# Optimization experiments

Hardware: AMD Instinct MI355X
Metric: run time of the kernel (lower is better)

## Reference

```python
import jax, jax.numpy as jnp
import numpy as np

B, D, H, W = 32, 64, 32, 32   # batch, laten_dim, latent spatial dims
K = 2048                      # codebook_size


def setup_inputs() -> dict:
    key = jax.random.key(0)
    k1, k2 = jax.random.split(key)
    laten = jax.random.normal(k1, (B, D, H, W), dtype=jnp.float32)
    codebook = jax.random.normal(k2, (K, D), dtype=jnp.float32)
    return {"laten": laten, "codebook": codebook}


def reference(laten, codebook):
    # Faithful jax translation of VQVAE.quant_laten.
    b, c, h, w = laten.shape
    # (b, c, h, w) -> (b*h*w, c)
    x = jnp.transpose(laten, (0, 2, 3, 1)).reshape(-1, c)  # (N, D)
    # avoids materializing the (N, K, D) broadcast intermediate.
    x_sq = jnp.sum(x * x, axis=-1, keepdims=True)          # (N, 1)
    e_sq = jnp.sum(codebook * codebook, axis=-1)           # (K,)
    l2_distance = (x_sq - 2.0 * (x @ codebook.T) + e_sq) / c  # (N, K)
    closest_idx_2d = jnp.argmin(l2_distance, axis=-1).reshape(b, h, w)
    # gather + permute(0, 3, 1, 2)
    quant_laten = jnp.transpose(codebook[closest_idx_2d], (0, 3, 1, 2))
    return closest_idx_2d, quant_laten
```

## Files before the change

### kernel.cpp

```cpp
#include <hip/hip_runtime.h>

#define N_PIX 32768
#define DIM   64
#define KCODE 2048

typedef __attribute__((ext_vector_type(8))) short bf16x8;
typedef __attribute__((ext_vector_type(4))) float f32x4;

__device__ inline unsigned short f2bf(float v) {
    unsigned int u = __float_as_uint(v);
    return (unsigned short)((u + 0x7FFFu + ((u >> 16) & 1u)) >> 16);
}
__device__ inline float bf2f(unsigned short b) {
    return __uint_as_float(((unsigned int)b) << 16);
}

__global__ __launch_bounds__(256)
void convert_b_kernel(const float* __restrict__ cb, unsigned short* __restrict__ Bg,
                      float* __restrict__ esq) {
    const int t   = blockIdx.x * 256 + threadIdx.x;
    const int n   = t >> 4;
    const int sub = t & 15;
    const int ntile = n >> 4, ni = n & 15;

    const float4 v = *(const float4*)(cb + (size_t)n * DIM + sub * 4);

    unsigned int h01, h23, m01, m23, l01, l23;
    {
        unsigned short h, m, l;
        float r1;
        h = f2bf(v.x); r1 = v.x - bf2f(h); m = f2bf(r1); l = f2bf(r1 - bf2f(m));
        h01 = h;       m01 = m;       l01 = l;
        h = f2bf(v.y); r1 = v.y - bf2f(h); m = f2bf(r1); l = f2bf(r1 - bf2f(m));
        h01 |= (unsigned int)h << 16; m01 |= (unsigned int)m << 16; l01 |= (unsigned int)l << 16;
        h = f2bf(v.z); r1 = v.z - bf2f(h); m = f2bf(r1); l = f2bf(r1 - bf2f(m));
        h23 = h;       m23 = m;       l23 = l;
        h = f2bf(v.w); r1 = v.w - bf2f(h); m = f2bf(r1); l = f2bf(r1 - bf2f(m));
        h23 |= (unsigned int)h << 16; m23 |= (unsigned int)m << 16; l23 |= (unsigned int)l << 16;
    }

    float s = (v.x * v.x + v.y * v.y) + (v.z * v.z + v.w * v.w);
#pragma unroll
    for (int mk = 1; mk < 16; mk <<= 1) s += __shfl_xor(s, mk, 16);
    if (sub == 0) esq[n] = s;

    char* outb = (char*)Bg;
    const size_t u = ((((size_t)ntile) * 8 + (sub >> 1)) << 8) + ni * 16 + (sub & 1) * 8;
    uint2 hw2 = {h01, h23}, mw2 = {m01, m23}, lw2 = {l01, l23};
    *(uint2*)(outb + u)          = hw2;
    *(uint2*)(outb + 262144 + u) = mw2;
    *(uint2*)(outb + 524288 + u) = lw2;
}

#define DO_PASS(APL, BPL)                                                    \
    _Pragma("unroll") for (int ks = 0; ks < 2; ++ks)                         \
    _Pragma("unroll") for (int mt = 0; mt < 2; ++mt)                         \
        acc[mt] = __builtin_amdgcn_mfma_f32_16x16x32_bf16(                   \
            af[APL][mt][ks], bfr[BPL][ks], acc[mt], 0, 0, 0);

#define LOAD_BFR(PL)                                                         \
    _Pragma("unroll") for (int ks = 0; ks < 2; ++ks)                         \
        bfr[PL][ks] = *(const bf16x8*)(rb + (PL) * 8192 + ks * 1024 + lane * 16);

__device__ __forceinline__ void stage_unit(const char* BgB, char* ringBase,
                                           int u, int it, int slotOff, int lane) {
    const int pl = u >> 3, rem = u & 7, g = rem >> 1, ks = rem & 1;
    const char* gsrc = BgB + (size_t)pl * 262144 + (size_t)(g * 32 + it) * 2048
                     + ks * 1024 + lane * 16;
    char* ldst = ringBase + slotOff + pl * 8192 + g * 2048 + ks * 1024;
    __builtin_amdgcn_global_load_lds(
        (const __attribute__((address_space(1))) void*)gsrc,
        (__attribute__((address_space(3))) void*)ldst, 16, 0, 0);
}

__global__ __launch_bounds__(512, 4)
void dist_fused_kernel(const float* __restrict__ laten,
                       const unsigned short* __restrict__ Bg,
                       const float* __restrict__ esq,
                       const float* __restrict__ cb,
                       float* __restrict__ out0, float* __restrict__ out1) {
    __shared__ __align__(16) char ring[49152];
    __shared__ float esqS[2048];

    const int tid  = threadIdx.x;
    const int lane = tid & 63;
    const int wave = tid >> 6;
    const int wm   = wave & 1;
    const int wn   = wave >> 1;
    const int quad = lane >> 4, col = lane & 15;
    const int bx = blockIdx.x;
    const int bb = bx >> 4, hw0 = (bx & 15) * 64;

    const char* BgB = (const char*)Bg;

    {
        const int p = tid & 63, dg = tid >> 6;
        const float* srcA = laten + (size_t)bb * 65536 + (size_t)dg * 8192 + hw0 + p;
        const int mt = p >> 4, mi = p & 15;
        alignas(16) unsigned short hv[8], mv[8], lv[8];
#pragma unroll
        for (int j = 0; j < 8; ++j) {
            float v = srcA[(size_t)j << 10];
            unsigned short h = f2bf(v);
            float r1 = v - bf2f(h);
            unsigned short m = f2bf(r1);
            unsigned short l = f2bf(r1 - bf2f(m));
            hv[j] = h; mv[j] = m; lv[j] = l;
        }
        int u = ((mt * 8 + dg) << 8) + mi * 16;
        *(uint4*)(ring + u)         = *(uint4*)hv;
        *(uint4*)(ring + 8192 + u)  = *(uint4*)mv;
        *(uint4*)(ring + 16384 + u) = *(uint4*)lv;
    }
    *(float4*)(esqS + tid * 4) = *(const float4*)(esq + tid * 4);
    __syncthreads();

    bf16x8 af[3][2][2];
#pragma unroll
    for (int pl = 0; pl < 3; ++pl)
#pragma unroll
        for (int mt = 0; mt < 2; ++mt)
#pragma unroll
            for (int ks = 0; ks < 2; ++ks)
                af[pl][mt][ks] = *(const bf16x8*)(ring + pl * 8192
                    + (((wm * 2 + mt) * 8 + ks * 4 + quad) << 8) + col * 16);
    __syncthreads();

    stage_unit(BgB, ring, wave,      0, 0, lane);
    stage_unit(BgB, ring, wave + 8,  0, 0, lane);
    stage_unit(BgB, ring, wave + 16, 0, 0, lane);
    __syncthreads();

    float best[2][4];
    int   bidx[2][4];
#pragma unroll
    for (int mt = 0; mt < 2; ++mt)
#pragma unroll
        for (int r = 0; r < 4; ++r) { best[mt][r] = 3.4e38f; bidx[mt][r] = 0; }

    for (int it = 0; it < 32; ++it) {
        if (it < 31) {
            const int slotOff = ((it + 1) & 1) * 24576;
            stage_unit(BgB, ring, wave,      it + 1, slotOff, lane);
            stage_unit(BgB, ring, wave + 8,  it + 1, slotOff, lane);
            stage_unit(BgB, ring, wave + 16, it + 1, slotOff, lane);
        }

        const char* rb = ring + (it & 1) * 24576 + wn * 2048;
        bf16x8 bfr[3][2];
        LOAD_BFR(2)
        LOAD_BFR(0)
        LOAD_BFR(1)

        f32x4 acc[2];
#pragma unroll
        for (int mt = 0; mt < 2; ++mt) acc[mt] = {0.f, 0.f, 0.f, 0.f};

        DO_PASS(0, 2)
        DO_PASS(2, 0)
        DO_PASS(1, 1)
        DO_PASS(0, 1)
        DO_PASS(1, 0)
        DO_PASS(0, 0)

        const int n = wn * 512 + it * 16 + col;
        const float e = esqS[n];
#pragma unroll
        for (int mt = 0; mt < 2; ++mt)
#pragma unroll
            for (int r = 0; r < 4; ++r) {
                float d = fmaf(-2.f, acc[mt][r], e);
                if (d < best[mt][r]) { best[mt][r] = d; bidx[mt][r] = n; }
            }

        __syncthreads();
    }

    float* redD = (float*)ring;
    int*   redI = (int*)(ring + 1024);
    int*   idxF = (int*)(ring + 2048);
#pragma unroll
    for (int mt = 0; mt < 2; ++mt)
#pragma unroll
        for (int r = 0; r < 4; ++r) {
            float d = best[mt][r];
            int   i = bidx[mt][r];
#pragma unroll
            for (int m = 1; m < 16; m <<= 1) {
                float od = __shfl_xor(d, m, 16);
                int   oi = __shfl_xor(i, m, 16);
                if (od < d || (od == d && oi < i)) { d = od; i = oi; }
            }
            if (col == 0) {
                int row = wm * 32 + mt * 16 + quad * 4 + r;
                redD[row * 4 + wn] = d;
                redI[row * 4 + wn] = i;
            }
        }
    __syncthreads();

    if (tid < 64) {
        float bd = redD[tid * 4]; int bi = redI[tid * 4];
#pragma unroll
        for (int w = 1; w < 4; ++w) {
            float d = redD[tid * 4 + w]; int i = redI[tid * 4 + w];
            if (d < bd || (d == bd && i < bi)) { bd = d; bi = i; }
        }
        out0[bx * 64 + tid] = (float)bi;
        idxF[tid] = bi;
    }
    __syncthreads();

    const int p = tid & 63, dg = tid >> 6;
    const int idx = idxF[p];
    const float4* srcr = (const float4*)(cb + ((size_t)idx << 6) + dg * 8);
    float* o = out1 + (size_t)bb * 65536 + (size_t)dg * 8192 + hw0 + p;
    float4 v0 = srcr[0], v1 = srcr[1];
    o[(size_t)0 << 10] = v0.x; o[(size_t)1 << 10] = v0.y;
    o[(size_t)2 << 10] = v0.z; o[(size_t)3 << 10] = v0.w;
    o[(size_t)4 << 10] = v1.x; o[(size_t)5 << 10] = v1.y;
    o[(size_t)6 << 10] = v1.z; o[(size_t)7 << 10] = v1.w;
}

extern "C" void kernel_launch(void* const* d_in, const int* in_sizes, int n_in,
                              void* d_out, int out_size, void* d_ws, size_t ws_size,
                              hipStream_t stream) {
    const float* laten = (const float*)d_in[0];
    const float* cb    = (const float*)d_in[1];

    float* out0 = (float*)d_out;
    float* out1 = (float*)d_out + N_PIX;

    float* esq = (float*)d_ws;
    unsigned short* Bg = (unsigned short*)(esq + 2048);

    convert_b_kernel<<<128, 256, 0, stream>>>(cb, Bg, esq);

    dist_fused_kernel<<<512, 512, 0, stream>>>(laten, Bg, esq, cb, out0, out1);
}
```

Baseline: 103.3 us.

## Triple-buffer codebook LDS ring with vmcnt waits and MFMA priority

Expands the LDS staging ring from two to three slots and prefetches two iterations ahead. Each iteration now waits only on the older async global-to-LDS loads with a partial vmcnt instead of a full barrier drain, and raises wave priority around the MFMA block. The goal is to hide global load latency behind matrix work. LDS per block grows from about 56KB to 80KB, which may lower the number of blocks resident per CU.

```diff
diff --git a/kernel.cpp b/kernel.cpp
--- a/kernel.cpp
+++ b/kernel.cpp
@@ -73,13 +73,52 @@
         (__attribute__((address_space(3))) void*)ldst, 16, 0, 0);
 }
 
+#define ITER(J, DOSTAGE, VM)                                                 \
+  {                                                                          \
+    if (DOSTAGE) {                                                           \
+      const int so2 = (((J) + 2) % 3) * 24576;                               \
+      stage_unit(BgB, ring, wave,      (J) + 2, so2, lane);                  \
+      stage_unit(BgB, ring, wave + 8,  (J) + 2, so2, lane);                  \
+      stage_unit(BgB, ring, wave + 16, (J) + 2, so2, lane);                  \
+    }                                                                        \
+    asm volatile("s_waitcnt vmcnt(" #VM ")" ::: "memory");                   \
+    __builtin_amdgcn_s_barrier();                                            \
+    asm volatile("" ::: "memory");                                           \
+    const char* rb = ring + (((J) % 3) * 24576) + wn * 2048;                 \
+    bf16x8 bfr[3][2];                                                        \
+    LOAD_BFR(2)                                                              \
+    LOAD_BFR(0)                                                              \
+    LOAD_BFR(1)                                                              \
+    f32x4 acc[2];                                                            \
+    acc[0] = f32x4{0.f, 0.f, 0.f, 0.f};                                      \
+    acc[1] = f32x4{0.f, 0.f, 0.f, 0.f};                                      \
+    __builtin_amdgcn_s_setprio(1);                                           \
+    DO_PASS(0, 2)                                                            \
+    DO_PASS(2, 0)                                                            \
+    DO_PASS(1, 1)                                                            \
+    DO_PASS(0, 1)                                                            \
+    DO_PASS(1, 0)                                                            \
+    DO_PASS(0, 0)                                                            \
+    __builtin_amdgcn_s_setprio(0);                                           \
+    const int n = wn * 512 + (J) * 16 + col;                                 \
+    const float e = esqS[n];                                                 \
+    _Pragma("unroll") for (int mt = 0; mt < 2; ++mt)                         \
+    _Pragma("unroll") for (int r = 0; r < 4; ++r) {                          \
+      float d = fmaf(-2.f, acc[mt][r], e);                                   \
+      if (d < best[mt][r]) { best[mt][r] = d; bidx[mt][r] = n; }             \
+    }                                                                        \
+    asm volatile("s_waitcnt lgkmcnt(0)" ::: "memory");                       \
+    __builtin_amdgcn_s_barrier();                                            \
+    asm volatile("" ::: "memory");                                           \
+  }
+
 __global__ __launch_bounds__(512, 4)
 void dist_fused_kernel(const float* __restrict__ laten,
                        const unsigned short* __restrict__ Bg,
                        const float* __restrict__ esq,
                        const float* __restrict__ cb,
                        float* __restrict__ out0, float* __restrict__ out1) {
-    __shared__ __align__(16) char ring[49152];
+    __shared__ __align__(16) char ring[73728];
     __shared__ float esqS[2048];
 
     const int tid  = threadIdx.x;
@@ -129,7 +168,9 @@
     stage_unit(BgB, ring, wave,      0, 0, lane);
     stage_unit(BgB, ring, wave + 8,  0, 0, lane);
     stage_unit(BgB, ring, wave + 16, 0, 0, lane);
-    __syncthreads();
+    stage_unit(BgB, ring, wave,      1, 24576, lane);
+    stage_unit(BgB, ring, wave + 8,  1, 24576, lane);
+    stage_unit(BgB, ring, wave + 16, 1, 24576, lane);
 
     float best[2][4];
     int   bidx[2][4];
@@ -138,43 +179,9 @@
 #pragma unroll
         for (int r = 0; r < 4; ++r) { best[mt][r] = 3.4e38f; bidx[mt][r] = 0; }
 
-    for (int it = 0; it < 32; ++it) {
-        if (it < 31) {
-            const int slotOff = ((it + 1) & 1) * 24576;
-            stage_unit(BgB, ring, wave,      it + 1, slotOff, lane);
-            stage_unit(BgB, ring, wave + 8,  it + 1, slotOff, lane);
-            stage_unit(BgB, ring, wave + 16, it + 1, slotOff, lane);
-        }
-
-        const char* rb = ring + (it & 1) * 24576 + wn * 2048;
-        bf16x8 bfr[3][2];
-        LOAD_BFR(2)
-        LOAD_BFR(0)
-        LOAD_BFR(1)
-
-        f32x4 acc[2];
-#pragma unroll
-        for (int mt = 0; mt < 2; ++mt) acc[mt] = {0.f, 0.f, 0.f, 0.f};
-
-        DO_PASS(0, 2)
-        DO_PASS(2, 0)
-        DO_PASS(1, 1)
-        DO_PASS(0, 1)
-        DO_PASS(1, 0)
-        DO_PASS(0, 0)
-
-        const int n = wn * 512 + it * 16 + col;
-        const float e = esqS[n];
-#pragma unroll
-        for (int mt = 0; mt < 2; ++mt)
-#pragma unroll
-            for (int r = 0; r < 4; ++r) {
-                float d = fmaf(-2.f, acc[mt][r], e);
-                if (d < best[mt][r]) { best[mt][r] = d; bidx[mt][r] = n; }
-            }
-
-        __syncthreads();
-    }
+    for (int it = 0; it < 30; ++it) ITER(it, true, 6)
+    ITER(30, false, 3)
+    ITER(31, false, 0)
 
     float* redD = (float*)ring;
     int*   redI = (int*)(ring + 1024);
```

Result: slower. 106.2 us (+2.8%).
